# Kernel optimization log

Measured on AMD Instinct MI355X. Metric: run time of the kernel, lower is better.

Reference implementation:

```python
import jax, jax.numpy as jnp
import numpy as np

N_BRANCH, N_LAYER = 4, 3
B, T, D_IN = 4, 1024, 32
D_MODEL, D_INNER, D_STATE, D_CONV, DT_RANK = 128, 256, 16, 4, 8
EMBED = 64
MAX_NORM = 10.0  # safe_expmap0 tangent-norm clip
EPS = 1e-7


def setup_inputs() -> dict:
    key = jax.random.key(0)
    ks = jax.random.split(key, 12)
    def nrm(k, shp, s=0.02):
        return s * jax.random.normal(k, shp, dtype=jnp.float32)
    A_init = jnp.log(jnp.arange(1, D_STATE + 1, dtype=jnp.float32))
    return {
        "trend": jax.random.normal(ks[0], (B, T, D_IN), jnp.float32),
        "seasonal_coarse": jax.random.normal(ks[1], (B, T, D_IN), jnp.float32),
        "seasonal_fine": jax.random.normal(ks[2], (B, T, D_IN), jnp.float32),
        "residual": jax.random.normal(ks[3], (B, T, D_IN), jnp.float32),
        "W_ip": nrm(ks[4], (N_BRANCH, D_IN, D_MODEL)),
        "b_ip": jnp.zeros((N_BRANCH, D_MODEL), jnp.float32),
        "W_in": nrm(ks[5], (N_BRANCH, N_LAYER, D_MODEL, 2 * D_INNER)),
        "conv_w": nrm(ks[6], (N_BRANCH, N_LAYER, D_INNER, D_CONV), 0.1),
        "conv_b": jnp.zeros((N_BRANCH, N_LAYER, D_INNER), jnp.float32),
        "W_x": nrm(ks[7], (N_BRANCH, N_LAYER, D_INNER, DT_RANK + 2 * D_STATE)),
        "W_dt": nrm(ks[8], (N_BRANCH, N_LAYER, DT_RANK, D_INNER), 0.1),
        "b_dt": jnp.full((N_BRANCH, N_LAYER, D_INNER), -4.6, jnp.float32),  # softplus ~ 0.01
        "A_log": jnp.broadcast_to(A_init, (N_BRANCH, N_LAYER, D_INNER, D_STATE)),
        "D_param": jnp.ones((N_BRANCH, N_LAYER, D_INNER), jnp.float32),
        "W_out": nrm(ks[9], (N_BRANCH, N_LAYER, D_INNER, D_MODEL)),
        "W_op": nrm(ks[10], (N_BRANCH, D_MODEL, EMBED)),
        "b_op": jnp.zeros((N_BRANCH, EMBED), jnp.float32),
        "eff_scale": jnp.asarray(0.1, jnp.float32),
    }


def _mamba_layer(x, Win, cw, cb, Wx, Wdt, bdt, Alog, Dp, Wout):
    # x: [B, T, d_model]
    Tlen = x.shape[1]
    xz = x @ Win                                   # [B,T,2*di]
    xp, z = jnp.split(xz, 2, axis=-1)
    # causal depthwise conv1d, kernel D_CONV
    xpad = jnp.pad(xp, ((0, 0), (D_CONV - 1, 0), (0, 0)))
    xc = sum(xpad[:, k:k + Tlen, :] * cw[:, k] for k in range(D_CONV))
    xc = jax.nn.silu(xc + cb)                      # [B,T,di]
    dbl = xc @ Wx                                  # [B,T,r+2s]
    dt = jax.nn.softplus(dbl[..., :DT_RANK] @ Wdt + bdt)   # [B,T,di]
    Bm = dbl[..., DT_RANK:DT_RANK + D_STATE]       # [B,T,s]
    Cm = dbl[..., DT_RANK + D_STATE:]              # [B,T,s]
    A = -jnp.exp(Alog)                             # [di,s]
    dA = jnp.exp(dt[..., None] * A)                # [B,T,di,s]
    dBx = (dt * xc)[..., None] * Bm[:, :, None, :] # [B,T,di,s]

    def step(h, inp):
        dA_t, dBx_t, C_t = inp
        h = dA_t * h + dBx_t
        return h, jnp.einsum('bds,bs->bd', h, C_t)

    h0 = jnp.zeros((x.shape[0], D_INNER, D_STATE), x.dtype)
    _, ys = jax.lax.scan(step, h0, (jnp.swapaxes(dA, 0, 1),
                                     jnp.swapaxes(dBx, 0, 1),
                                     jnp.swapaxes(Cm, 0, 1)))
    y = jnp.swapaxes(ys, 0, 1) + Dp * xc
    return (y * jax.nn.silu(z)) @ Wout


def _embed(x, Wip, bip, Wins, cws, cbs, Wxs, Wdts, bdts, Alogs, Dps, Wouts, Wop, bop):
    h = x @ Wip + bip
    for l in range(N_LAYER):
        h = _mamba_layer(h, Wins[l], cws[l], cbs[l], Wxs[l], Wdts[l], bdts[l],
                         Alogs[l], Dps[l], Wouts[l])
    return h.mean(axis=1) @ Wop + bop              # [B, EMBED]


def _expmap0(v):
    # safe expmap0 on Lorentz (k=1): clip tangent norm at MAX_NORM
    n = jnp.linalg.norm(v, axis=-1, keepdims=True)
    nc = jnp.clip(n, EPS, MAX_NORM)
    v = v * (nc / jnp.maximum(n, EPS))
    return jnp.concatenate([jnp.cosh(nc), jnp.sinh(nc) / nc * v], axis=-1)


def _projx(x):
    sp = x[..., 1:]
    t = jnp.sqrt(1.0 + jnp.sum(sp * sp, axis=-1, keepdims=True))
    return jnp.concatenate([t, sp], axis=-1)


def _logmap0(x):
    sp = x[..., 1:]
    t = jnp.maximum(x[..., :1], 1.0 + EPS)
    d = jnp.arccosh(t)
    spn = jnp.maximum(jnp.linalg.norm(sp, axis=-1, keepdims=True), EPS)
    return d * sp / spn


def _forward(trend, seasonal_coarse, seasonal_fine, residual,
             W_ip, b_ip, W_in, conv_w, conv_b, W_x, W_dt, b_dt,
             A_log, D_param, W_out, W_op, b_op, eff_scale):
    xs = [trend, seasonal_coarse, seasonal_fine, residual]
    z_t = [
        _embed(xs[b], W_ip[b], b_ip[b], W_in[b], conv_w[b], conv_b[b], W_x[b],
               W_dt[b], b_dt[b], A_log[b], D_param[b], W_out[b], W_op[b], b_op[b])
        for b in range(N_BRANCH)
    ]
    es = jnp.tanh(eff_scale)
    z_h = [_projx(_expmap0(z * es)) for z in z_t]
    us = [_logmap0(zh) for zh in z_h]
    combined_tangent = us[0] + us[1] + us[2] + us[3]
    combined_h = _projx(_expmap0(combined_tangent * es))
    return (*z_t, *z_h, combined_tangent, combined_h)


def reference(trend, seasonal_coarse, seasonal_fine, residual,
              W_ip, b_ip, W_in, conv_w, conv_b, W_x, W_dt, b_dt,
              A_log, D_param, W_out, W_op, b_op, eff_scale):
    return _forward(trend, seasonal_coarse, seasonal_fine, residual,
                    W_ip, b_ip, W_in, conv_w, conv_b, W_x, W_dt, b_dt,
                    A_log, D_param, W_out, W_op, b_op, eff_scale)
```

## Files before the change

kernel.cpp:

```cpp
#include <hip/hip_runtime.h>
#include <math.h>

#define NBR 4
#define NLAY 3
#define Bk 4
#define Tk 1024
#define DIN 32
#define DMODEL 128
#define DINNER 256
#define DSTATE 16
#define DTRANK 8
#define EMBEDk 64
#define BT (Bk*Tk)
#define EPSF 1e-7f
#define MAXNF 10.0f
#define LCH 64
#define NCH (Tk/LCH)
#define UF 8
#define NWB 320

typedef __bf16 bf16x8 __attribute__((ext_vector_type(8)));
typedef float  f32x4  __attribute__((ext_vector_type(4)));
typedef unsigned short u16x8 __attribute__((ext_vector_type(8)));
typedef unsigned short u16x4 __attribute__((ext_vector_type(4)));

__device__ __forceinline__ float siluf(float x){ return x / (1.f + __expf(-x)); }
__device__ __forceinline__ float softplusf(float x){ return (x > 20.f) ? x : log1pf(__expf(x)); }
__device__ __forceinline__ unsigned short f2b(float x){
    union { float f; unsigned u; } v; v.f = x;
    unsigned r = v.u + 0x7FFF + ((v.u >> 16) & 1);
    return (unsigned short)(r >> 16);
}
__device__ __forceinline__ float b2f(unsigned short u){
    union { unsigned u; float f; } v; v.u = ((unsigned)u) << 16; return v.f;
}

__device__ __forceinline__ void gll16(const void* g, void* l){
    __builtin_amdgcn_global_load_lds(
        (const __attribute__((address_space(1))) unsigned int*)g,
        (__attribute__((address_space(3))) unsigned int*)l,
        16, 0, 0);
}

__device__ __forceinline__ void dA_pow(float q, float* dA){
    dA[0] = q;             dA[1] = q * q;
    dA[2] = dA[1] * dA[0]; dA[3] = dA[1] * dA[1];
    dA[4] = dA[3] * dA[0]; dA[5] = dA[3] * dA[1];
    dA[6] = dA[3] * dA[2]; dA[7] = dA[3] * dA[3];
    #pragma unroll
    for (int s = 8; s < 16; ++s) dA[s] = dA[s - 8] * dA[7];
}
__device__ __forceinline__ void dA_exp(float dtv, const float* Aa, float* dA){
    #pragma unroll
    for (int s = 0; s < 16; ++s) dA[s] = __expf(dtv * Aa[s]);
}

template<int MODE>
__global__ __launch_bounds__(256) void bgemm_k(
    const unsigned short* __restrict__ Ab, long aBr, int K,
    const unsigned short* __restrict__ Bt, long bBr,
    float* __restrict__ C0, long c0Br,
    float* __restrict__ C1, long c1Br,
    unsigned short* __restrict__ Cb, long cbBr,
    const float* __restrict__ bias, long biasBr)
{
    const int br = blockIdx.z;
    Ab += (long)br * aBr;
    Bt += (long)br * bBr;
    if (MODE == 3) C0 += (long)br * c0Br;
    if (MODE == 0 || MODE == 3) C1 += (long)br * c1Br;
    if (MODE == 0) Cb += (long)br * cbBr;
    if (MODE == 3) bias += (long)br * biasBr;
    const int m0 = blockIdx.x * 64, n0 = blockIdx.y * 64;
    __shared__ __align__(16) unsigned short As[8 * 64 * 8];
    __shared__ __align__(16) unsigned short Bs[8 * 64 * 8];
    const int tid = threadIdx.x;
    const int lane = tid & 63, w = tid >> 6;
    const int wm = w >> 1, wn = w & 1;
    const int quad = lane >> 4, l15 = lane & 15;
    f32x4 acc00 = {0,0,0,0}, acc01 = {0,0,0,0}, acc10 = {0,0,0,0}, acc11 = {0,0,0,0};
    for (int kc = 0; kc < K; kc += 64) {
        #pragma unroll
        for (int it = 0; it < 2; ++it) {
            const int kch = w + it * 4;
            gll16(Ab + (long)(m0 + lane) * K + kc + kch * 8, &As[(kch * 64) * 8]);
            gll16(Bt + (long)(n0 + lane) * K + kc + kch * 8, &Bs[(kch * 64) * 8]);
        }
        __syncthreads();
        #pragma unroll
        for (int k0 = 0; k0 < 64; k0 += 32) {
            const int kch = (k0 >> 3) + quad;
            bf16x8 a0 = *(const bf16x8*)&As[(kch * 64 + wm * 32 +      l15) * 8];
            bf16x8 a1 = *(const bf16x8*)&As[(kch * 64 + wm * 32 + 16 + l15) * 8];
            bf16x8 b0 = *(const bf16x8*)&Bs[(kch * 64 + wn * 32 +      l15) * 8];
            bf16x8 b1 = *(const bf16x8*)&Bs[(kch * 64 + wn * 32 + 16 + l15) * 8];
            acc00 = __builtin_amdgcn_mfma_f32_16x16x32_bf16(a0, b0, acc00, 0, 0, 0);
            acc01 = __builtin_amdgcn_mfma_f32_16x16x32_bf16(a0, b1, acc01, 0, 0, 0);
            acc10 = __builtin_amdgcn_mfma_f32_16x16x32_bf16(a1, b0, acc10, 0, 0, 0);
            acc11 = __builtin_amdgcn_mfma_f32_16x16x32_bf16(a1, b1, acc11, 0, 0, 0);
        }
        __syncthreads();
    }
    #pragma unroll
    for (int e = 0; e < 4; ++e) {
        f32x4 a = (e == 0) ? acc00 : (e == 1) ? acc01 : (e == 2) ? acc10 : acc11;
        const int msub = (e >> 1) * 16, nsub = (e & 1) * 16;
        const int col = n0 + wn * 32 + nsub + l15;
        #pragma unroll
        for (int r = 0; r < 4; ++r) {
            const int row = m0 + wm * 32 + msub + quad * 4 + r;
            const float v = a[r];
            if (MODE == 0) {
                if (n0 < 256) Cb[(long)row * 256 + col] = f2b(v);
                else          C1[(long)row * 256 + (col - 256)] = siluf(v);
            } else {
                if (col < 256)      C0[(long)row * 256 + col] = softplusf(v + bias[col]);
                else if (col < 288) C1[(long)row * 32 + (col - 256)] = v;
            }
        }
    }
}

__global__ __launch_bounds__(256) void sgemmWT_k(
    const float* __restrict__ Wout, const float* __restrict__ Win,
    const float* __restrict__ Wip, const float* __restrict__ bip,
    const float* __restrict__ Wop,
    unsigned short* __restrict__ WfT, float* __restrict__ Weq,
    float* __restrict__ Wcomb)
{
    const int z = blockIdx.z;
    const int tid = threadIdx.x;
    const int tx = tid & 15, ty = tid >> 4;
    __shared__ float As_[32][68];
    __shared__ float Bs_[32][68];
    float acc[4][4] = {};
    if (z < 8) {
        const int p = z >> 2, br = z & 3;
        const float* A  = Wout + (long)(br * NLAY + p) * DINNER * DMODEL;
        const float* Bw = Win  + (long)(br * NLAY + p + 1) * DMODEL * 512;
        const int m0 = blockIdx.x * 64, n0 = blockIdx.y * 64;
        for (int kc = 0; kc < DMODEL; kc += 32) {
            #pragma unroll
            for (int it = 0; it < 2; ++it) {
                int id = tid + it * 256;
                int r = id >> 3, c4 = (id & 7) << 2;
                float4 v = *(const float4*)(A + (long)(m0 + r) * DMODEL + kc + c4);
                As_[c4+0][r] = v.x; As_[c4+1][r] = v.y; As_[c4+2][r] = v.z; As_[c4+3][r] = v.w;
                int rb = id >> 4, cb = (id & 15) << 2;
                *(float4*)&Bs_[rb][cb] = *(const float4*)(Bw + (long)(kc + rb) * 512 + n0 + cb);
            }
            __syncthreads();
            #pragma unroll
            for (int kk = 0; kk < 32; ++kk) {
                float4 a4 = *(const float4*)&As_[kk][ty << 2];
                float4 b4 = *(const float4*)&Bs_[kk][tx << 2];
                float av[4] = {a4.x, a4.y, a4.z, a4.w};
                float bv[4] = {b4.x, b4.y, b4.z, b4.w};
                #pragma unroll
                for (int i = 0; i < 4; ++i)
                    #pragma unroll
                    for (int j = 0; j < 4; ++j)
                        acc[i][j] = fmaf(av[i], bv[j], acc[i][j]);
            }
            __syncthreads();
        }
        unsigned short* o = WfT + (long)z * 512 * 256;
        const int row0 = m0 + (ty << 2), col = n0 + (tx << 2);
        #pragma unroll
        for (int j = 0; j < 4; ++j) {
            u16x4 v;
            #pragma unroll
            for (int i = 0; i < 4; ++i) v[i] = f2b(acc[i][j]);
            *(u16x4*)(o + (long)(col + j) * 256 + row0) = v;
        }
    } else if (z == 8) {
        const int br = blockIdx.x;
        const float* A  = Wip + (long)br * DIN * DMODEL;
        const float* bp = bip + (long)br * DMODEL;
        const float* Bw = Win + (long)br * NLAY * DMODEL * 512;
        const int n0 = blockIdx.y * 64;
        for (int kc = 0; kc < DMODEL; kc += 32) {
            #pragma unroll
            for (int it = 0; it < 2; ++it) {
                int id = tid + it * 256;
                int r = id >> 3, c4 = (id & 7) << 2;
                float4 v;
                if (r < 32)       v = *(const float4*)(A + (long)r * DMODEL + kc + c4);
                else if (r == 32) v = *(const float4*)(bp + kc + c4);
                else              { v.x = 0.f; v.y = 0.f; v.z = 0.f; v.w = 0.f; }
                As_[c4+0][r] = v.x; As_[c4+1][r] = v.y; As_[c4+2][r] = v.z; As_[c4+3][r] = v.w;
                int rb = id >> 4, cb = (id & 15) << 2;
                *(float4*)&Bs_[rb][cb] = *(const float4*)(Bw + (long)(kc + rb) * 512 + n0 + cb);
            }
            __syncthreads();
            #pragma unroll
            for (int kk = 0; kk < 32; ++kk) {
                float4 a4 = *(const float4*)&As_[kk][ty << 2];
                float4 b4 = *(const float4*)&Bs_[kk][tx << 2];
                float av[4] = {a4.x, a4.y, a4.z, a4.w};
                float bv[4] = {b4.x, b4.y, b4.z, b4.w};
                #pragma unroll
                for (int i = 0; i < 4; ++i)
                    #pragma unroll
                    for (int j = 0; j < 4; ++j)
                        acc[i][j] = fmaf(av[i], bv[j], acc[i][j]);
            }
            __syncthreads();
        }
        float* C = Weq + (long)br * 33 * 512;
        const int col = n0 + (tx << 2);
        #pragma unroll
        for (int i = 0; i < 4; ++i) {
            const int row = (ty << 2) + i;
            if (row < 33) {
                float4 v4; v4.x = acc[i][0]; v4.y = acc[i][1]; v4.z = acc[i][2]; v4.w = acc[i][3];
                *(float4*)(C + (long)row * 512 + col) = v4;
            }
        }
    } else {
        if (blockIdx.y >= 4) return;
        const int br = blockIdx.y;
        const float* A  = Wout + (long)(br * NLAY + 2) * DINNER * DMODEL;
        const float* Bw = Wop  + (long)br * DMODEL * EMBEDk;
        const int m0 = blockIdx.x * 64;
        for (int kc = 0; kc < DMODEL; kc += 32) {
            #pragma unroll
            for (int it = 0; it < 2; ++it) {
                int id = tid + it * 256;
                int r = id >> 3, c4 = (id & 7) << 2;
                float4 v = *(const float4*)(A + (long)(m0 + r) * DMODEL + kc + c4);
                As_[c4+0][r] = v.x; As_[c4+1][r] = v.y; As_[c4+2][r] = v.z; As_[c4+3][r] = v.w;
                int rb = id >> 4, cb = (id & 15) << 2;
                if (cb < 64)
                    *(float4*)&Bs_[rb][cb] = *(const float4*)(Bw + (long)(kc + rb) * EMBEDk + cb);
            }
            __syncthreads();
            #pragma unroll
            for (int kk = 0; kk < 32; ++kk) {
                float4 a4 = *(const float4*)&As_[kk][ty << 2];
                float4 b4 = *(const float4*)&Bs_[kk][tx << 2];
                float av[4] = {a4.x, a4.y, a4.z, a4.w};
                float bv[4] = {b4.x, b4.y, b4.z, b4.w};
                #pragma unroll
                for (int i = 0; i < 4; ++i)
                    #pragma unroll
                    for (int j = 0; j < 4; ++j)
                        acc[i][j] = fmaf(av[i], bv[j], acc[i][j]);
            }
            __syncthreads();
        }
        float* C = Wcomb + (long)br * DINNER * EMBEDk;
        const int col = tx << 2;
        #pragma unroll
        for (int i = 0; i < 4; ++i) {
            const int row = m0 + (ty << 2) + i;
            float4 v4; v4.x = acc[i][0]; v4.y = acc[i][1]; v4.z = acc[i][2]; v4.w = acc[i][3];
            *(float4*)(C + (long)row * EMBEDk + col) = v4;
        }
    }
}

__global__ __launch_bounds__(256) void prepC_k(
    const float* __restrict__ Wx, const float* __restrict__ Wdt,
    unsigned short* __restrict__ o)
{
    const int n = blockIdx.x, bl = blockIdx.y;
    const int k = threadIdx.x;
    const float* WxP = Wx + (long)bl * DINNER * 40;
    float v;
    if (n < 256) {
        const float* WdtP = Wdt + (long)bl * DTRANK * DINNER;
        float s = 0.f;
        #pragma unroll
        for (int r = 0; r < 8; ++r) s = fmaf(WxP[k * 40 + r], WdtP[r * DINNER + n], s);
        v = s;
    } else if (n < 288) {
        v = WxP[k * 40 + 8 + (n - 256)];
    } else {
        v = 0.f;
    }
    o[(long)bl * NWB * DINNER + (long)n * DINNER + k] = f2b(v);
}

__global__ __launch_bounds__(256) void xgemm0_k(
    const float* __restrict__ A0, const float* __restrict__ A1,
    const float* __restrict__ A2, const float* __restrict__ A3,
    const float* __restrict__ Weq,
    float* __restrict__ zb, unsigned short* __restrict__ xpb)
{
    const int br = blockIdx.z;
    const float* A = (br == 1) ? A1 : (br == 2) ? A2 : (br == 3) ? A3 : A0;
    const float* W = Weq + (long)br * 33 * 512;
    float* C1 = zb + (long)br * BT * DINNER;
    unsigned short* Cb = xpb + (long)br * BT * DINNER;
    const int m0 = blockIdx.x * 64, n0 = blockIdx.y * 64;
    __shared__ float As_[32][68];
    __shared__ float Bs_[32][68];
    const int tid = threadIdx.x;
    const int tx = tid & 15, ty = tid >> 4;
    float acc[4][4] = {};
    {
        #pragma unroll
        for (int it = 0; it < 2; ++it) {
            int id = tid + it * 256;
            int r = id >> 3, c4 = (id & 7) << 2;
            float4 v = *(const float4*)(A + (long)(m0 + r) * DIN + c4);
            As_[c4+0][r] = v.x; As_[c4+1][r] = v.y; As_[c4+2][r] = v.z; As_[c4+3][r] = v.w;
            int rb = id >> 4, cb = (id & 15) << 2;
            *(float4*)&Bs_[rb][cb] = *(const float4*)(W + (long)rb * 512 + n0 + cb);
        }
        __syncthreads();
        #pragma unroll
        for (int kk = 0; kk < 32; ++kk) {
            float4 a4 = *(const float4*)&As_[kk][ty << 2];
            float4 b4 = *(const float4*)&Bs_[kk][tx << 2];
            float av[4] = {a4.x, a4.y, a4.z, a4.w};
            float bv[4] = {b4.x, b4.y, b4.z, b4.w};
            #pragma unroll
            for (int i = 0; i < 4; ++i)
                #pragma unroll
                for (int j = 0; j < 4; ++j)
                    acc[i][j] = fmaf(av[i], bv[j], acc[i][j]);
        }
    }
    const int col = n0 + (tx << 2);
    float be[4];
    #pragma unroll
    for (int j = 0; j < 4; ++j) be[j] = W[32 * 512 + col + j];
    #pragma unroll
    for (int i = 0; i < 4; ++i) {
        const int row = m0 + (ty << 2) + i;
        #pragma unroll
        for (int j = 0; j < 4; ++j) {
            const float v = acc[i][j] + be[j];
            if (n0 < 256) Cb[(long)row * 256 + col + j] = f2b(v);
            else          C1[(long)row * 256 + (col - 256 + j)] = siluf(v);
        }
    }
}

__global__ __launch_bounds__(256) void conv_k(
    const unsigned short* __restrict__ xp, const float* __restrict__ cw,
    const float* __restrict__ cb, unsigned short* __restrict__ xcb, int layer)
{
    const int br = blockIdx.y;
    const long base = (long)br * BT * DINNER;
    const long idx8 = ((long)blockIdx.x * 256 + threadIdx.x) * 8;
    const int d0 = (int)(idx8 & (DINNER - 1));
    const long row = idx8 >> 8;
    const int t = (int)(row & (Tk - 1));
    const float* cwp = cw + ((long)(br * NLAY + layer) * DINNER + d0) * 4;
    const float* cbp = cb + (long)(br * NLAY + layer) * DINNER + d0;
    u16x8 in[4];
    #pragma unroll
    for (int k = 0; k < 4; ++k) {
        const int tt = t + k - 3;
        if (tt >= 0) {
            in[k] = *(const u16x8*)(xp + base + idx8 + (long)(k - 3) * DINNER);
        } else {
            #pragma unroll
            for (int j = 0; j < 8; ++j) in[k][j] = 0;
        }
    }
    u16x8 o;
    #pragma unroll
    for (int j = 0; j < 8; ++j) {
        float acc = cbp[j];
        #pragma unroll
        for (int k = 0; k < 4; ++k)
            acc = fmaf(b2f(in[k][j]), cwp[j * 4 + k], acc);
        o[j] = f2b(siluf(acc));
    }
    *(u16x8*)(xcb + base + idx8) = o;
}

__global__ __launch_bounds__(256) void scan1_k(
    const float* __restrict__ dtb, const unsigned short* __restrict__ xcb,
    const float* __restrict__ bcb, const float* __restrict__ Alog,
    float* __restrict__ recbuf, int layer)
{
    const int c = blockIdx.x, b = blockIdx.y, br = blockIdx.z;
    const int d = threadIdx.x;
    const float* Ap = Alog + ((long)(br * NLAY + layer) * DINNER + d) * DSTATE;
    float Aa[16];
    bool pw = true;
    #pragma unroll
    for (int s = 0; s < 16; ++s) {
        Aa[s] = -__expf(Ap[s]);
        pw = pw && (fabsf(Aa[s] + (float)(s + 1)) < 1e-3f);
    }
    const long rbase = (long)br * BT + (long)b * Tk + (long)c * LCH;
    const float* dtp = dtb + rbase * DINNER + d;
    const unsigned short* xcp = xcb + rbase * DINNER + d;
    __shared__ float bcs[LCH * 32];
    {
        const float4* g = (const float4*)(bcb + rbase * 32);
        float4* l = (float4*)bcs;
        l[d] = g[d]; l[d + 256] = g[d + 256];
    }
    float dtc[UF], xcc[UF];
    #pragma unroll
    for (int u = 0; u < UF; ++u) {
        dtc[u] = dtp[(long)u * DINNER];
        xcc[u] = b2f(xcp[(long)u * DINNER]);
    }
    __syncthreads();
    float h[16];
    #pragma unroll
    for (int s = 0; s < 16; ++s) h[s] = 0.f;
    float sumdt = 0.f;
    for (int base = 0; base < LCH; base += UF) {
        const int nb = (base + UF < LCH) ? base + UF : base;
        float dtn[UF], xcn[UF];
        #pragma unroll
        for (int u = 0; u < UF; ++u) {
            dtn[u] = dtp[(long)(nb + u) * DINNER];
            xcn[u] = b2f(xcp[(long)(nb + u) * DINNER]);
        }
        #pragma unroll
        for (int u = 0; u < UF; ++u) {
            const int t = base + u;
            const float dtv = dtc[u];
            const float dtxc = dtv * xcc[u];
            sumdt += dtv;
            float dA[16];
            if (pw) dA_pow(__expf(-dtv), dA);
            else    dA_exp(dtv, Aa, dA);
            const float* bcT = bcs + t * 32;
            #pragma unroll
            for (int s = 0; s < 16; ++s)
                h[s] = fmaf(dA[s], h[s], dtxc * bcT[s]);
        }
        #pragma unroll
        for (int u = 0; u < UF; ++u) { dtc[u] = dtn[u]; xcc[u] = xcn[u]; }
    }
    float* sb = recbuf + (((long)(br * 4 + b) * (NCH - 1) + c) * 17) * 256 + d;
    #pragma unroll
    for (int s = 0; s < 16; ++s) sb[s * 256] = h[s];
    sb[16 * 256] = sumdt;
}

__global__ __launch_bounds__(256) void scan3_k(
    const float* __restrict__ dtb, const unsigned short* __restrict__ xcb,
    const float* __restrict__ bcb, const float* __restrict__ zb,
    const float* __restrict__ Alog, const float* __restrict__ Dpar,
    const float* __restrict__ recbuf, unsigned short* __restrict__ yzb, int layer)
{
    const int c = blockIdx.x, b = blockIdx.y, br = blockIdx.z;
    const int d = threadIdx.x;
    const float* Ap = Alog + ((long)(br * NLAY + layer) * DINNER + d) * DSTATE;
    float Aa[16];
    bool pw = true;
    #pragma unroll
    for (int s = 0; s < 16; ++s) {
        Aa[s] = -__expf(Ap[s]);
        pw = pw && (fabsf(Aa[s] + (float)(s + 1)) < 1e-3f);
    }
    float h[16];
    #pragma unroll
    for (int s = 0; s < 16; ++s) h[s] = 0.f;
    if (c > 0) {
        const float* recB = recbuf + ((long)(br * 4 + b) * (NCH - 1)) * 17 * 256 + d;
        float rh[16], rs;
        #pragma unroll
        for (int s = 0; s < 16; ++s) rh[s] = recB[s * 256];
        rs = recB[16 * 256];
        for (int cc = 0; cc < c; ++cc) {
            float nh[16], ns = 0.f;
            if (cc + 1 < c) {
                const float* r2 = recB + (long)(cc + 1) * 17 * 256;
                #pragma unroll
                for (int s = 0; s < 16; ++s) nh[s] = r2[s * 256];
                ns = r2[16 * 256];
            } else {
                #pragma unroll
                for (int s = 0; s < 16; ++s) nh[s] = 0.f;
            }
            float P[16];
            if (pw) dA_pow(__expf(-rs), P);
            else    dA_exp(rs, Aa, P);
            #pragma unroll
            for (int s = 0; s < 16; ++s) h[s] = fmaf(h[s], P[s], rh[s]);
            #pragma unroll
            for (int s = 0; s < 16; ++s) rh[s] = nh[s];
            rs = ns;
        }
    }
    const float Dp = Dpar[(br * NLAY + layer) * DINNER + d];
    const long rbase = (long)br * BT + (long)b * Tk + (long)c * LCH;
    const float* dtp = dtb + rbase * DINNER + d;
    const unsigned short* xcp = xcb + rbase * DINNER + d;
    const float* zp  = zb  + rbase * DINNER + d;
    unsigned short* yp = yzb + rbase * DINNER + d;
    __shared__ float bcs[LCH * 32];
    {
        const float4* g = (const float4*)(bcb + rbase * 32);
        float4* l = (float4*)bcs;
        l[d] = g[d]; l[d + 256] = g[d + 256];
    }
    float dtc[UF], xcc[UF], zc[UF];
    #pragma unroll
    for (int u = 0; u < UF; ++u) {
        dtc[u] = dtp[(long)u * DINNER];
        xcc[u] = b2f(xcp[(long)u * DINNER]);
        zc[u]  = zp[(long)u * DINNER];
    }
    __syncthreads();
    for (int base = 0; base < LCH; base += UF) {
        const int nb = (base + UF < LCH) ? base + UF : base;
        float dtn[UF], xcn[UF], zn[UF];
        #pragma unroll
        for (int u = 0; u < UF; ++u) {
            dtn[u] = dtp[(long)(nb + u) * DINNER];
            xcn[u] = b2f(xcp[(long)(nb + u) * DINNER]);
            zn[u]  = zp[(long)(nb + u) * DINNER];
        }
        #pragma unroll
        for (int u = 0; u < UF; ++u) {
            const int t = base + u;
            const float dtv = dtc[u], xcv = xcc[u];
            const float dtxc = dtv * xcv;
            float dA[16];
            if (pw) dA_pow(__expf(-dtv), dA);
            else    dA_exp(dtv, Aa, dA);
            const float* bcT = bcs + t * 32;
            #pragma unroll
            for (int s = 0; s < 16; ++s)
                h[s] = fmaf(dA[s], h[s], dtxc * bcT[s]);
            float y0 = 0.f, y1 = 0.f, y2 = 0.f, y3 = 0.f;
            #pragma unroll
            for (int s = 0; s < 16; s += 4) {
                y0 = fmaf(h[s+0], bcT[16+s+0], y0);
                y1 = fmaf(h[s+1], bcT[16+s+1], y1);
                y2 = fmaf(h[s+2], bcT[16+s+2], y2);
                y3 = fmaf(h[s+3], bcT[16+s+3], y3);
            }
            const float y = (y0 + y1) + (y2 + y3) + Dp * xcv;
            yp[(long)t * DINNER] = f2b(y * zc[u]);
        }
        #pragma unroll
        for (int u = 0; u < UF; ++u) { dtc[u] = dtn[u]; xcc[u] = xcn[u]; zc[u] = zn[u]; }
    }
}

__global__ __launch_bounds__(256) void csum1_k(
    const unsigned short* __restrict__ yz, float* __restrict__ part)
{
    const int ch = blockIdx.x, brb = blockIdx.y;
    const int br = brb >> 2, b = brb & 3;
    const long rbase = (long)br * BT + (long)b * Tk + (long)ch * 128;
    const int tid = threadIdx.x;
    const int cg = tid & 31;
    const int ro = tid >> 5;
    const unsigned short* p = yz + (rbase + ro) * DINNER + cg * 8;
    float acc[8] = {0,0,0,0,0,0,0,0};
    for (int it = 0; it < 16; ++it) {
        u16x8 v = *(const u16x8*)(p + (long)it * 8 * DINNER);
        #pragma unroll
        for (int j = 0; j < 8; ++j) acc[j] += b2f(v[j]);
    }
    __shared__ float sm[8][256];
    #pragma unroll
    for (int j = 0; j < 8; ++j) sm[ro][cg * 8 + j] = acc[j];
    __syncthreads();
    float s = 0.f;
    #pragma unroll
    for (int r = 0; r < 8; ++r) s += sm[r][tid];
    part[((long)brb * 8 + ch) * 256 + tid] = s;
}

__global__ __launch_bounds__(256) void csum2_k(
    const float* __restrict__ part, const float* __restrict__ Wcomb,
    const float* __restrict__ bop, float* __restrict__ outzt)
{
    const int brb = blockIdx.x, br = brb >> 2;
    const int tid = threadIdx.x;
    __shared__ float vm[256];
    __shared__ float red[4][64];
    float s = 0.f;
    #pragma unroll
    for (int ch = 0; ch < 8; ++ch) s += part[((long)brb * 8 + ch) * 256 + tid];
    vm[tid] = s * (1.0f / Tk);
    __syncthreads();
    const float* Wc = Wcomb + (long)br * DINNER * EMBEDk;
    const int col = tid & 63, seg = tid >> 6;
    float a = 0.f;
    #pragma unroll 8
    for (int k = seg * 64; k < seg * 64 + 64; ++k)
        a = fmaf(vm[k], Wc[(long)k * EMBEDk + col], a);
    red[seg][col] = a;
    __syncthreads();
    if (tid < 64)
        outzt[brb * EMBEDk + tid] =
            red[0][tid] + red[1][tid] + red[2][tid] + red[3][tid] + bop[br * EMBEDk + tid];
}

__global__ __launch_bounds__(64) void final_k(
    const float* __restrict__ zt, float* __restrict__ out, const float* __restrict__ eff)
{
    const float es = tanhf(eff[0]);
    __shared__ float us[NBR][Bk][EMBEDk];
    const int t = threadIdx.x;
    if (t < 16) {
        const int br = t >> 2, b = t & 3;
        const float* z = zt + br * (Bk * EMBEDk) + b * EMBEDk;
        float n2 = 0.f;
        for (int e = 0; e < EMBEDk; ++e) { float v = z[e] * es; n2 = fmaf(v, v, n2); }
        const float n  = sqrtf(n2);
        const float nc = fminf(fmaxf(n, EPSF), MAXNF);
        const float sc = nc / fmaxf(n, EPSF);
        const float sh = sinhf(nc) / nc;
        const float fac = es * sc * sh;
        float* zh = out + 1024 + br * (Bk * (EMBEDk + 1)) + b * (EMBEDk + 1);
        float sp2 = 0.f;
        for (int e = 0; e < EMBEDk; ++e) {
            float spv = z[e] * fac;
            sp2 = fmaf(spv, spv, sp2);
            zh[1 + e] = spv;
            us[br][b][e] = spv;
        }
        const float t0 = sqrtf(1.f + sp2);
        zh[0] = t0;
        const float dd  = acoshf(fmaxf(t0, 1.f + EPSF));
        const float spn = fmaxf(sqrtf(sp2), EPSF);
        const float rr  = dd / spn;
        for (int e = 0; e < EMBEDk; ++e) us[br][b][e] *= rr;
    }
    __syncthreads();
    if (t < 4) {
        const int b = t;
        float ct[EMBEDk];
        float* cto = out + 2064 + b * EMBEDk;
        for (int e = 0; e < EMBEDk; ++e) {
            float v = us[0][b][e] + us[1][b][e] + us[2][b][e] + us[3][b][e];
            ct[e] = v; cto[e] = v;
        }
        float n2 = 0.f;
        for (int e = 0; e < EMBEDk; ++e) { float v = ct[e] * es; n2 = fmaf(v, v, n2); }
        const float n  = sqrtf(n2);
        const float nc = fminf(fmaxf(n, EPSF), MAXNF);
        const float sc = nc / fmaxf(n, EPSF);
        const float sh = sinhf(nc) / nc;
        const float fac = es * sc * sh;
        float* ch = out + 2320 + b * (EMBEDk + 1);
        float sp2 = 0.f;
        for (int e = 0; e < EMBEDk; ++e) {
            float spv = ct[e] * fac;
            sp2 = fmaf(spv, spv, sp2);
            ch[1 + e] = spv;
        }
        ch[0] = sqrtf(1.f + sp2);
    }
}

extern "C" void kernel_launch(void* const* d_in, const int* in_sizes, int n_in,
                              void* d_out, int out_size, void* d_ws, size_t ws_size,
                              hipStream_t stream)
{
    const float* X0 = (const float*)d_in[0];
    const float* X1 = (const float*)d_in[1];
    const float* X2 = (const float*)d_in[2];
    const float* X3 = (const float*)d_in[3];
    const float* W_ip   = (const float*)d_in[4];
    const float* b_ip   = (const float*)d_in[5];
    const float* W_in   = (const float*)d_in[6];
    const float* conv_w = (const float*)d_in[7];
    const float* conv_b = (const float*)d_in[8];
    const float* W_x    = (const float*)d_in[9];
    const float* W_dt   = (const float*)d_in[10];
    const float* b_dt   = (const float*)d_in[11];
    const float* A_log  = (const float*)d_in[12];
    const float* D_par  = (const float*)d_in[13];
    const float* W_out  = (const float*)d_in[14];
    const float* W_op   = (const float*)d_in[15];
    const float* b_op   = (const float*)d_in[16];
    const float* eff    = (const float*)d_in[17];
    float* out = (float*)d_out;
    float* ws  = (float*)d_ws;

    float* buf_z  = ws;
    float* buf_dt = buf_z  + (long)NBR * BT * DINNER;
    float* buf_bc = buf_dt + (long)NBR * BT * DINNER;
    float* part   = buf_bc + (long)NBR * BT * 32;
    float* recbuf = part   + 32768;
    float* Weq    = recbuf + (long)16 * (NCH - 1) * 17 * 256;
    float* Wcomb  = Weq + 4 * 33 * 512;
    unsigned short* xp_bf = (unsigned short*)(Wcomb + 4 * 256 * 64);
    unsigned short* xc_bf = xp_bf + (long)NBR * BT * DINNER;
    unsigned short* yz_bf = xc_bf + (long)NBR * BT * DINNER;
    unsigned short* WfT   = yz_bf + (long)NBR * BT * DINNER;
    unsigned short* WcT   = WfT   + (long)8 * 512 * DINNER;

    prepC_k<<<dim3(NWB, NBR * NLAY), 256, 0, stream>>>(W_x, W_dt, WcT);
    sgemmWT_k<<<dim3(4, 8, 10), 256, 0, stream>>>(
        W_out, W_in, W_ip, b_ip, W_op, WfT, Weq, Wcomb);

    xgemm0_k<<<dim3(BT / 64, 8, NBR), 256, 0, stream>>>(
        X0, X1, X2, X3, Weq, buf_z, xp_bf);

    for (int l = 0; l < NLAY; ++l) {
        if (l > 0) {
            bgemm_k<0><<<dim3(BT / 64, 8, NBR), 256, 0, stream>>>(
                yz_bf, (long)BT * DINNER, DINNER,
                WfT + (long)(l - 1) * 4 * 512 * DINNER, (long)512 * DINNER,
                nullptr, 0, buf_z, (long)BT * DINNER,
                xp_bf, (long)BT * DINNER, nullptr, 0);
        }
        conv_k<<<dim3((BT * DINNER) / (256 * 8), NBR), 256, 0, stream>>>(
            xp_bf, conv_w, conv_b, xc_bf, l);
        bgemm_k<3><<<dim3(BT / 64, NWB / 64, NBR), 256, 0, stream>>>(
            xc_bf, (long)BT * DINNER, DINNER,
            WcT + (long)l * NWB * DINNER, (long)NLAY * NWB * DINNER,
            buf_dt, (long)BT * DINNER, buf_bc, (long)BT * 32,
            nullptr, 0, b_dt + l * DINNER, (long)NLAY * DINNER);
        scan1_k<<<dim3(NCH - 1, Bk, NBR), 256, 0, stream>>>(
            buf_dt, xc_bf, buf_bc, A_log, recbuf, l);
        scan3_k<<<dim3(NCH, Bk, NBR), 256, 0, stream>>>(
            buf_dt, xc_bf, buf_bc, buf_z, A_log, D_par, recbuf, yz_bf, l);
    }

    csum1_k<<<dim3(8, 16), 256, 0, stream>>>(yz_bf, part);
    csum2_k<<<16, 256, 0, stream>>>(part, Wcomb, b_op, out);
    final_k<<<1, 64, 0, stream>>>(out, out, eff);
}
```

Baseline: 429.9 us.

## Store dt and z in bf16 and split scan state across two threads per channel

The dt and gate z intermediates are now written as bf16 instead of fp32, which halves their memory traffic in the GEMM epilogues and the scan kernels. The scan kernels now run 512 threads per block, with each channel's 16 SSM states split across two lanes of 8. The two partial y sums are combined with a shuffle. This doubles thread parallelism and reduces per-thread registers, at the cost of extra precision loss in dt and z and duplicated loads of dt, xc and z per lane pair.

```diff
diff --git a/kernel.cpp b/kernel.cpp
--- a/kernel.cpp
+++ b/kernel.cpp
@@ -42,35 +42,30 @@
         16, 0, 0);
 }
 
-__device__ __forceinline__ void dA_pow(float q, float* dA){
-    dA[0] = q;             dA[1] = q * q;
-    dA[2] = dA[1] * dA[0]; dA[3] = dA[1] * dA[1];
-    dA[4] = dA[3] * dA[0]; dA[5] = dA[3] * dA[1];
-    dA[6] = dA[3] * dA[2]; dA[7] = dA[3] * dA[3];
-    #pragma unroll
-    for (int s = 8; s < 16; ++s) dA[s] = dA[s - 8] * dA[7];
-}
-__device__ __forceinline__ void dA_exp(float dtv, const float* Aa, float* dA){
-    #pragma unroll
-    for (int s = 0; s < 16; ++s) dA[s] = __expf(dtv * Aa[s]);
+__device__ __forceinline__ void dA_pow8(float q, int sh, float* dA){
+    const float q2 = q * q, q4 = q2 * q2, q8 = q4 * q4;
+    const float f = sh ? q8 : 1.0f;
+    dA[0] = q * f;       dA[1] = q2 * f;
+    dA[2] = q2 * q * f;  dA[3] = q4 * f;
+    dA[4] = q4 * q * f;  dA[5] = q4 * q2 * f;
+    dA[6] = q4 * q2 * q * f; dA[7] = q8 * f;
 }
 
 template<int MODE>
 __global__ __launch_bounds__(256) void bgemm_k(
     const unsigned short* __restrict__ Ab, long aBr, int K,
     const unsigned short* __restrict__ Bt, long bBr,
-    float* __restrict__ C0, long c0Br,
-    float* __restrict__ C1, long c1Br,
-    unsigned short* __restrict__ Cb, long cbBr,
+    unsigned short* __restrict__ Cu0, long cu0Br,
+    unsigned short* __restrict__ Cu1, long cu1Br,
+    float* __restrict__ Cf, long cfBr,
     const float* __restrict__ bias, long biasBr)
 {
     const int br = blockIdx.z;
     Ab += (long)br * aBr;
     Bt += (long)br * bBr;
-    if (MODE == 3) C0 += (long)br * c0Br;
-    if (MODE == 0 || MODE == 3) C1 += (long)br * c1Br;
-    if (MODE == 0) Cb += (long)br * cbBr;
-    if (MODE == 3) bias += (long)br * biasBr;
+    Cu0 += (long)br * cu0Br;
+    if (MODE == 0) Cu1 += (long)br * cu1Br;
+    if (MODE == 3) { Cf += (long)br * cfBr; bias += (long)br * biasBr; }
     const int m0 = blockIdx.x * 64, n0 = blockIdx.y * 64;
     __shared__ __align__(16) unsigned short As[8 * 64 * 8];
     __shared__ __align__(16) unsigned short Bs[8 * 64 * 8];
@@ -111,11 +106,11 @@
             const int row = m0 + wm * 32 + msub + quad * 4 + r;
             const float v = a[r];
             if (MODE == 0) {
-                if (n0 < 256) Cb[(long)row * 256 + col] = f2b(v);
-                else          C1[(long)row * 256 + (col - 256)] = siluf(v);
+                if (n0 < 256) Cu0[(long)row * 256 + col] = f2b(v);
+                else          Cu1[(long)row * 256 + (col - 256)] = f2b(siluf(v));
             } else {
-                if (col < 256)      C0[(long)row * 256 + col] = softplusf(v + bias[col]);
-                else if (col < 288) C1[(long)row * 32 + (col - 256)] = v;
+                if (col < 256)      Cu0[(long)row * 256 + col] = f2b(softplusf(v + bias[col]));
+                else if (col < 288) Cf[(long)row * 32 + (col - 256)] = v;
             }
         }
     }
@@ -286,12 +281,12 @@
     const float* __restrict__ A0, const float* __restrict__ A1,
     const float* __restrict__ A2, const float* __restrict__ A3,
     const float* __restrict__ Weq,
-    float* __restrict__ zb, unsigned short* __restrict__ xpb)
+    unsigned short* __restrict__ zb, unsigned short* __restrict__ xpb)
 {
     const int br = blockIdx.z;
     const float* A = (br == 1) ? A1 : (br == 2) ? A2 : (br == 3) ? A3 : A0;
     const float* W = Weq + (long)br * 33 * 512;
-    float* C1 = zb + (long)br * BT * DINNER;
+    unsigned short* Cz = zb + (long)br * BT * DINNER;
     unsigned short* Cb = xpb + (long)br * BT * DINNER;
     const int m0 = blockIdx.x * 64, n0 = blockIdx.y * 64;
     __shared__ float As_[32][68];
@@ -334,7 +329,7 @@
         for (int j = 0; j < 4; ++j) {
             const float v = acc[i][j] + be[j];
             if (n0 < 256) Cb[(long)row * 256 + col + j] = f2b(v);
-            else          C1[(long)row * 256 + (col - 256 + j)] = siluf(v);
+            else          Cz[(long)row * 256 + (col - 256 + j)] = f2b(siluf(v));
         }
     }
 }
@@ -374,47 +369,43 @@
     *(u16x8*)(xcb + base + idx8) = o;
 }
 
-__global__ __launch_bounds__(256) void scan1_k(
-    const float* __restrict__ dtb, const unsigned short* __restrict__ xcb,
+__global__ __launch_bounds__(512) void scan1_k(
+    const unsigned short* __restrict__ dtb, const unsigned short* __restrict__ xcb,
     const float* __restrict__ bcb, const float* __restrict__ Alog,
     float* __restrict__ recbuf, int layer)
 {
     const int c = blockIdx.x, b = blockIdx.y, br = blockIdx.z;
-    const int d = threadIdx.x;
-    const float* Ap = Alog + ((long)(br * NLAY + layer) * DINNER + d) * DSTATE;
-    float Aa[16];
-    bool pw = true;
-    #pragma unroll
-    for (int s = 0; s < 16; ++s) {
-        Aa[s] = -__expf(Ap[s]);
-        pw = pw && (fabsf(Aa[s] + (float)(s + 1)) < 1e-3f);
+    const int tid = threadIdx.x;
+    const int d = tid >> 1, sh = tid & 1, s0 = sh << 3;
+    const float* Ap = Alog + ((long)(br * NLAY + layer) * DINNER + d) * DSTATE + s0;
+    float Aa[8]; bool pw = true;
+    #pragma unroll
+    for (int k = 0; k < 8; ++k) {
+        Aa[k] = -__expf(Ap[k]);
+        pw = pw && (fabsf(Aa[k] + (float)(s0 + k + 1)) < 1e-3f);
     }
     const long rbase = (long)br * BT + (long)b * Tk + (long)c * LCH;
-    const float* dtp = dtb + rbase * DINNER + d;
+    const unsigned short* dtp = dtb + rbase * DINNER + d;
     const unsigned short* xcp = xcb + rbase * DINNER + d;
     __shared__ float bcs[LCH * 32];
-    {
-        const float4* g = (const float4*)(bcb + rbase * 32);
-        float4* l = (float4*)bcs;
-        l[d] = g[d]; l[d + 256] = g[d + 256];
-    }
+    ((float4*)bcs)[tid] = ((const float4*)(bcb + rbase * 32))[tid];
     float dtc[UF], xcc[UF];
     #pragma unroll
     for (int u = 0; u < UF; ++u) {
-        dtc[u] = dtp[(long)u * DINNER];
+        dtc[u] = b2f(dtp[(long)u * DINNER]);
         xcc[u] = b2f(xcp[(long)u * DINNER]);
     }
     __syncthreads();
-    float h[16];
-    #pragma unroll
-    for (int s = 0; s < 16; ++s) h[s] = 0.f;
+    float h[8];
+    #pragma unroll
+    for (int k = 0; k < 8; ++k) h[k] = 0.f;
     float sumdt = 0.f;
     for (int base = 0; base < LCH; base += UF) {
         const int nb = (base + UF < LCH) ? base + UF : base;
         float dtn[UF], xcn[UF];
         #pragma unroll
         for (int u = 0; u < UF; ++u) {
-            dtn[u] = dtp[(long)(nb + u) * DINNER];
+            dtn[u] = b2f(dtp[(long)(nb + u) * DINNER]);
             xcn[u] = b2f(xcp[(long)(nb + u) * DINNER]);
         }
         #pragma unroll
@@ -423,87 +414,89 @@
             const float dtv = dtc[u];
             const float dtxc = dtv * xcc[u];
             sumdt += dtv;
-            float dA[16];
-            if (pw) dA_pow(__expf(-dtv), dA);
-            else    dA_exp(dtv, Aa, dA);
-            const float* bcT = bcs + t * 32;
-            #pragma unroll
-            for (int s = 0; s < 16; ++s)
-                h[s] = fmaf(dA[s], h[s], dtxc * bcT[s]);
+            float dA[8];
+            if (pw) dA_pow8(__expf(-dtv), sh, dA);
+            else {
+                #pragma unroll
+                for (int k = 0; k < 8; ++k) dA[k] = __expf(dtv * Aa[k]);
+            }
+            const float* bcT = bcs + t * 32 + s0;
+            #pragma unroll
+            for (int k = 0; k < 8; ++k)
+                h[k] = fmaf(dA[k], h[k], dtxc * bcT[k]);
         }
         #pragma unroll
         for (int u = 0; u < UF; ++u) { dtc[u] = dtn[u]; xcc[u] = xcn[u]; }
     }
     float* sb = recbuf + (((long)(br * 4 + b) * (NCH - 1) + c) * 17) * 256 + d;
     #pragma unroll
-    for (int s = 0; s < 16; ++s) sb[s * 256] = h[s];
-    sb[16 * 256] = sumdt;
-}
-
-__global__ __launch_bounds__(256) void scan3_k(
-    const float* __restrict__ dtb, const unsigned short* __restrict__ xcb,
-    const float* __restrict__ bcb, const float* __restrict__ zb,
+    for (int k = 0; k < 8; ++k) sb[(s0 + k) * 256] = h[k];
+    if (!sh) sb[16 * 256] = sumdt;
+}
+
+__global__ __launch_bounds__(512) void scan3_k(
+    const unsigned short* __restrict__ dtb, const unsigned short* __restrict__ xcb,
+    const float* __restrict__ bcb, const unsigned short* __restrict__ zb,
     const float* __restrict__ Alog, const float* __restrict__ Dpar,
     const float* __restrict__ recbuf, unsigned short* __restrict__ yzb, int layer)
 {
     const int c = blockIdx.x, b = blockIdx.y, br = blockIdx.z;
-    const int d = threadIdx.x;
-    const float* Ap = Alog + ((long)(br * NLAY + layer) * DINNER + d) * DSTATE;
-    float Aa[16];
-    bool pw = true;
-    #pragma unroll
-    for (int s = 0; s < 16; ++s) {
-        Aa[s] = -__expf(Ap[s]);
-        pw = pw && (fabsf(Aa[s] + (float)(s + 1)) < 1e-3f);
-    }
-    float h[16];
-    #pragma unroll
-    for (int s = 0; s < 16; ++s) h[s] = 0.f;
+    const int tid = threadIdx.x;
+    const int d = tid >> 1, sh = tid & 1, s0 = sh << 3;
+    const float* Ap = Alog + ((long)(br * NLAY + layer) * DINNER + d) * DSTATE + s0;
+    float Aa[8]; bool pw = true;
+    #pragma unroll
+    for (int k = 0; k < 8; ++k) {
+        Aa[k] = -__expf(Ap[k]);
+        pw = pw && (fabsf(Aa[k] + (float)(s0 + k + 1)) < 1e-3f);
+    }
+    float h[8];
+    #pragma unroll
+    for (int k = 0; k < 8; ++k) h[k] = 0.f;
     if (c > 0) {
         const float* recB = recbuf + ((long)(br * 4 + b) * (NCH - 1)) * 17 * 256 + d;
-        float rh[16], rs;
-        #pragma unroll
-        for (int s = 0; s < 16; ++s) rh[s] = recB[s * 256];
+        float rh[8], rs;
+        #pragma unroll
+        for (int k = 0; k < 8; ++k) rh[k] = recB[(s0 + k) * 256];
         rs = recB[16 * 256];
         for (int cc = 0; cc < c; ++cc) {
-            float nh[16], ns = 0.f;
+            float nh[8], ns = 0.f;
             if (cc + 1 < c) {
                 const float* r2 = recB + (long)(cc + 1) * 17 * 256;
                 #pragma unroll
-                for (int s = 0; s < 16; ++s) nh[s] = r2[s * 256];
+                for (int k = 0; k < 8; ++k) nh[k] = r2[(s0 + k) * 256];
                 ns = r2[16 * 256];
             } else {
                 #pragma unroll
-                for (int s = 0; s < 16; ++s) nh[s] = 0.f;
-            }
-            float P[16];
-            if (pw) dA_pow(__expf(-rs), P);
-            else    dA_exp(rs, Aa, P);
-            #pragma unroll
-            for (int s = 0; s < 16; ++s) h[s] = fmaf(h[s], P[s], rh[s]);
-            #pragma unroll
-            for (int s = 0; s < 16; ++s) rh[s] = nh[s];
+                for (int k = 0; k < 8; ++k) nh[k] = 0.f;
+            }
+            float P[8];
+            if (pw) dA_pow8(__expf(-rs), sh, P);
+            else {
+                #pragma unroll
+                for (int k = 0; k < 8; ++k) P[k] = __expf(rs * Aa[k]);
+            }
+            #pragma unroll
+            for (int k = 0; k < 8; ++k) h[k] = fmaf(h[k], P[k], rh[k]);
+            #pragma unroll
+            for (int k = 0; k < 8; ++k) rh[k] = nh[k];
             rs = ns;
         }
     }
     const float Dp = Dpar[(br * NLAY + layer) * DINNER + d];
     const long rbase = (long)br * BT + (long)b * Tk + (long)c * LCH;
-    const float* dtp = dtb + rbase * DINNER + d;
+    const unsigned short* dtp = dtb + rbase * DINNER + d;
     const unsigned short* xcp = xcb + rbase * DINNER + d;
-    const float* zp  = zb  + rbase * DINNER + d;
+    const unsigned short* zp  = zb  + rbase * DINNER + d;
     unsigned short* yp = yzb + rbase * DINNER + d;
     __shared__ float bcs[LCH * 32];
-    {
-        const float4* g = (const float4*)(bcb + rbase * 32);
-        float4* l = (float4*)bcs;
-        l[d] = g[d]; l[d + 256] = g[d + 256];
-    }
+    ((float4*)bcs)[tid] = ((const float4*)(bcb + rbase * 32))[tid];
     float dtc[UF], xcc[UF], zc[UF];
     #pragma unroll
     for (int u = 0; u < UF; ++u) {
-        dtc[u] = dtp[(long)u * DINNER];
+        dtc[u] = b2f(dtp[(long)u * DINNER]);
         xcc[u] = b2f(xcp[(long)u * DINNER]);
-        zc[u]  = zp[(long)u * DINNER];
+        zc[u]  = b2f(zp[(long)u * DINNER]);
     }
     __syncthreads();
     for (int base = 0; base < LCH; base += UF) {
@@ -511,32 +504,38 @@
         float dtn[UF], xcn[UF], zn[UF];
         #pragma unroll
         for (int u = 0; u < UF; ++u) {
-            dtn[u] = dtp[(long)(nb + u) * DINNER];
+            dtn[u] = b2f(dtp[(long)(nb + u) * DINNER]);
             xcn[u] = b2f(xcp[(long)(nb + u) * DINNER]);
-            zn[u]  = zp[(long)(nb + u) * DINNER];
+            zn[u]  = b2f(zp[(long)(nb + u) * DINNER]);
         }
         #pragma unroll
         for (int u = 0; u < UF; ++u) {
             const int t = base + u;
             const float dtv = dtc[u], xcv = xcc[u];
             const float dtxc = dtv * xcv;
-            float dA[16];
-            if (pw) dA_pow(__expf(-dtv), dA);
-            else    dA_exp(dtv, Aa, dA);
-            const float* bcT = bcs + t * 32;
-            #pragma unroll
-            for (int s = 0; s < 16; ++s)
-                h[s] = fmaf(dA[s], h[s], dtxc * bcT[s]);
-            float y0 = 0.f, y1 = 0.f, y2 = 0.f, y3 = 0.f;
-            #pragma unroll
-            for (int s = 0; s < 16; s += 4) {
-                y0 = fmaf(h[s+0], bcT[16+s+0], y0);
-                y1 = fmaf(h[s+1], bcT[16+s+1], y1);
-                y2 = fmaf(h[s+2], bcT[16+s+2], y2);
-                y3 = fmaf(h[s+3], bcT[16+s+3], y3);
-            }
-            const float y = (y0 + y1) + (y2 + y3) + Dp * xcv;
-            yp[(long)t * DINNER] = f2b(y * zc[u]);
+            float dA[8];
+            if (pw) dA_pow8(__expf(-dtv), sh, dA);
+            else {
+                #pragma unroll
+                for (int k = 0; k < 8; ++k) dA[k] = __expf(dtv * Aa[k]);
+            }
+            const float* bcT = bcs + t * 32 + s0;
+            #pragma unroll
+            for (int k = 0; k < 8; ++k)
+                h[k] = fmaf(dA[k], h[k], dtxc * bcT[k]);
+            float y0 = 0.f, y1 = 0.f;
+            const float* cT = bcs + t * 32 + 16 + s0;
+            #pragma unroll
+            for (int k = 0; k < 8; k += 2) {
+                y0 = fmaf(h[k+0], cT[k+0], y0);
+                y1 = fmaf(h[k+1], cT[k+1], y1);
+            }
+            const float yp_ = y0 + y1;
+            const float ytot = yp_ + __shfl_xor(yp_, 1);
+            if (!sh) {
+                const float y = ytot + Dp * xcv;
+                yp[(long)t * DINNER] = f2b(y * zc[u]);
+            }
         }
         #pragma unroll
         for (int u = 0; u < UF; ++u) { dtc[u] = dtn[u]; xcc[u] = xcn[u]; zc[u] = zn[u]; }
@@ -678,16 +677,16 @@
     float* out = (float*)d_out;
     float* ws  = (float*)d_ws;
 
-    float* buf_z  = ws;
-    float* buf_dt = buf_z  + (long)NBR * BT * DINNER;
-    float* buf_bc = buf_dt + (long)NBR * BT * DINNER;
+    float* buf_bc = ws;
     float* part   = buf_bc + (long)NBR * BT * 32;
-    float* recbuf = part   + 32768;
+    float* recbuf = part + 32768;
     float* Weq    = recbuf + (long)16 * (NCH - 1) * 17 * 256;
     float* Wcomb  = Weq + 4 * 33 * 512;
     unsigned short* xp_bf = (unsigned short*)(Wcomb + 4 * 256 * 64);
     unsigned short* xc_bf = xp_bf + (long)NBR * BT * DINNER;
-    unsigned short* yz_bf = xc_bf + (long)NBR * BT * DINNER;
+    unsigned short* z_bf  = xc_bf + (long)NBR * BT * DINNER;
+    unsigned short* dt_bf = z_bf  + (long)NBR * BT * DINNER;
+    unsigned short* yz_bf = dt_bf + (long)NBR * BT * DINNER;
     unsigned short* WfT   = yz_bf + (long)NBR * BT * DINNER;
     unsigned short* WcT   = WfT   + (long)8 * 512 * DINNER;
 
@@ -696,27 +695,30 @@
         W_out, W_in, W_ip, b_ip, W_op, WfT, Weq, Wcomb);
 
     xgemm0_k<<<dim3(BT / 64, 8, NBR), 256, 0, stream>>>(
-        X0, X1, X2, X3, Weq, buf_z, xp_bf);
+        X0, X1, X2, X3, Weq, z_bf, xp_bf);
 
     for (int l = 0; l < NLAY; ++l) {
         if (l > 0) {
             bgemm_k<0><<<dim3(BT / 64, 8, NBR), 256, 0, stream>>>(
                 yz_bf, (long)BT * DINNER, DINNER,
                 WfT + (long)(l - 1) * 4 * 512 * DINNER, (long)512 * DINNER,
-                nullptr, 0, buf_z, (long)BT * DINNER,
-                xp_bf, (long)BT * DINNER, nullptr, 0);
+                xp_bf, (long)BT * DINNER,
+                z_bf, (long)BT * DINNER,
+                nullptr, 0, nullptr, 0);
         }
         conv_k<<<dim3((BT * DINNER) / (256 * 8), NBR), 256, 0, stream>>>(
             xp_bf, conv_w, conv_b, xc_bf, l);
         bgemm_k<3><<<dim3(BT / 64, NWB / 64, NBR), 256, 0, stream>>>(
             xc_bf, (long)BT * DINNER, DINNER,
             WcT + (long)l * NWB * DINNER, (long)NLAY * NWB * DINNER,
-            buf_dt, (long)BT * DINNER, buf_bc, (long)BT * 32,
-            nullptr, 0, b_dt + l * DINNER, (long)NLAY * DINNER);
-        scan1_k<<<dim3(NCH - 1, Bk, NBR), 256, 0, stream>>>(
-            buf_dt, xc_bf, buf_bc, A_log, recbuf, l);
-        scan3_k<<<dim3(NCH, Bk, NBR), 256, 0, stream>>>(
-            buf_dt, xc_bf, buf_bc, buf_z, A_log, D_par, recbuf, yz_bf, l);
+            dt_bf, (long)BT * DINNER,
+            nullptr, 0,
+            buf_bc, (long)BT * 32,
+            b_dt + l * DINNER, (long)NLAY * DINNER);
+        scan1_k<<<dim3(NCH - 1, Bk, NBR), 512, 0, stream>>>(
+            dt_bf, xc_bf, buf_bc, A_log, recbuf, l);
+        scan3_k<<<dim3(NCH, Bk, NBR), 512, 0, stream>>>(
+            dt_bf, xc_bf, buf_bc, z_bf, A_log, D_par, recbuf, yz_bf, l);
     }
 
     csum1_k<<<dim3(8, 16), 256, 0, stream>>>(yz_bf, part);
```

Result: no change. 424.0 us (-1.4%).
